# Performance work log

Measured on AMD Instinct MI355X. Metric: run time of the kernel, lower is better.

The kernel has to match this reference:

```python
import jax, jax.numpy as jnp
import numpy as np

WINSIZE = 11
SIGMA = 1.5
L_RANGE = 1.0

def _gaussian_window(winsize, channel, dtype=jnp.float32):
    x = jnp.arange(winsize, dtype=dtype)
    g = jnp.exp(-((x - winsize // 2) ** 2) / (2.0 * SIGMA ** 2))
    g = g / g.sum()
    w2d = jnp.outer(g, g)                      # [ws, ws]
    # depthwise kernel [channel, 1, ws, ws] (OIHW, feature_group_count=channel)
    return jnp.broadcast_to(w2d, (channel, 1, winsize, winsize))

def _dwconv(x, w, channel):
    pad = WINSIZE // 2
    return jax.lax.conv_general_dilated(
        x, w, window_strides=(1, 1), padding=[(pad, pad), (pad, pad)],
        dimension_numbers=('NCHW', 'OIHW', 'NCHW'),
        feature_group_count=channel)

def _ssim(X, Y):
    channel = X.shape[1]
    w = _gaussian_window(WINSIZE, channel, X.dtype)
    mu1 = _dwconv(X, w, channel)
    mu2 = _dwconv(Y, w, channel)
    mu1_sq = mu1 * mu1
    mu2_sq = mu2 * mu2
    mu1_mu2 = mu1 * mu2
    sigma1_sq = _dwconv(X * X, w, channel) - mu1_sq
    sigma2_sq = _dwconv(Y * Y, w, channel) - mu2_sq
    sigma12 = _dwconv(X * Y, w, channel) - mu1_mu2
    C1 = (0.01 * L_RANGE) ** 2
    C2 = (0.03 * L_RANGE) ** 2
    ssim_map = ((2.0 * mu1_mu2 + C1) * (2.0 * sigma12 + C2)) / \
               ((mu1_sq + mu2_sq + C1) * (sigma1_sq + sigma2_sq + C2))
    return jnp.mean(ssim_map)  # sizeavg=True

def setup_inputs() -> dict:
    key = jax.random.key(0)
    k1, k2 = jax.random.split(key)
    shape = (16, 3, 512, 512)
    X = jax.random.uniform(k1, shape, dtype=jnp.float32)
    Y = jax.random.uniform(k2, shape, dtype=jnp.float32)
    return {"X": X, "Y": Y}

def reference(X, Y):
    return 1.0 - _ssim(X, Y)
```

## Files before the change

### kernel.cpp

```cpp
#include <hip/hip_runtime.h>
#include <hip/hip_fp16.h>


#define ROWS 32
#define NI   (ROWS + 10)
#define NBLOCKS (48 * 16)
#define NPIXEL 12582912.0

__global__ __launch_bounds__(256) void ssim_pk_kernel(
    const float* __restrict__ X, const float* __restrict__ Y,
    float* __restrict__ partial)
{
    __shared__ __half2 sb[2][2][2][262];

    const int tid = threadIdx.x;
    const int bid = blockIdx.x;
    const int img = bid >> 4;
    const int r0  = (bid & 15) * ROWS;

    const float* __restrict__ Xi = X + (size_t)img * (512 * 512);
    const float* __restrict__ Yi = Y + (size_t)img * (512 * 512);

    float g[11];
    {
        float s = 0.f;
        #pragma unroll
        for (int i = 0; i < 11; ++i) {
            float d = (float)(i - 5);
            float e = expf(-d * d * (1.0f / 4.5f));
            g[i] = e; s += e;
        }
        float inv = 1.0f / s;
        #pragma unroll
        for (int i = 0; i < 11; ++i) g[i] *= inv;
    }
    __half2 w2[11];
    #pragma unroll
    for (int i = 0; i < 11; ++i) w2[i] = __float2half2_rn(g[i]);

    const __half2 hz = __float2half2_rn(0.f);

    if (tid < 2) {
        #pragma unroll
        for (int b = 0; b < 2; ++b)
            #pragma unroll
            for (int m = 0; m < 2; ++m) {
                sb[b][m][0][1 + tid]   = hz;
                sb[b][m][0][259 + tid] = hz;
                sb[b][m][1][tid]       = hz;
                sb[b][m][1][259 + tid] = hz;
            }
    }

    const int c2 = 2 * tid;

    {
        int gr = r0 - 5;
        float2 xv = {0.f, 0.f}, yv = {0.f, 0.f};
        float xn = 0.f, yn = 0.f;
        if ((unsigned)gr < 512u) {
            const float* xr = Xi + (size_t)gr * 512;
            const float* yr = Yi + (size_t)gr * 512;
            xv = *(const float2*)(xr + c2);
            yv = *(const float2*)(yr + c2);
            if (tid < 255) { xn = xr[c2 + 2]; yn = yr[c2 + 2]; }
        }
        sb[0][0][0][tid + 3] = __floats2half2_rn(xv.x, xv.y);
        sb[0][0][1][tid + 3] = __floats2half2_rn(xv.y, xn);
        sb[0][1][0][tid + 3] = __floats2half2_rn(yv.x, yv.y);
        sb[0][1][1][tid + 3] = __floats2half2_rn(yv.y, yn);
        if (tid == 0) {
            sb[0][0][1][2] = __floats2half2_rn(0.f, xv.x);
            sb[0][1][1][2] = __floats2half2_rn(0.f, yv.x);
        }
    }
    __syncthreads();

    __half2 ring[5][11];
    float acc = 0.f;
    const float C1 = 1e-4f, C2 = 9e-4f;

    #pragma unroll 1
    for (int jb = 0; jb < 44; jb += 11) {
        #pragma unroll
        for (int ph = 0; ph < 11; ++ph) {
            int j = jb + ph;
            if (j < NI) {
                const int cur = j & 1, nxt = cur ^ 1;
                const int jn = j + 1;

                float2 nxv = {0.f, 0.f}, nyv = {0.f, 0.f};
                float nxn = 0.f, nyn = 0.f;
                if (jn < NI) {
                    int gr = r0 - 5 + jn;
                    if ((unsigned)gr < 512u) {
                        const float* xr = Xi + (size_t)gr * 512;
                        const float* yr = Yi + (size_t)gr * 512;
                        nxv = *(const float2*)(xr + c2);
                        nyv = *(const float2*)(yr + c2);
                        if (tid < 255) { nxn = xr[c2 + 2]; nyn = yr[c2 + 2]; }
                    }
                }

                {
                    const __half2* ex = &sb[cur][0][0][tid];
                    const __half2* ox = &sb[cur][0][1][tid];
                    const __half2* ey = &sb[cur][1][0][tid];
                    const __half2* oy = &sb[cur][1][1][tid];
                    __half2 hx = hz, hy = hz, hxx = hz, hyy = hz, hxy = hz;
                    #pragma unroll
                    for (int k = 0; k < 11; ++k) {
                        __half2 xk = (k & 1) ? ex[(k + 1) >> 1] : ox[k >> 1];
                        __half2 yk = (k & 1) ? ey[(k + 1) >> 1] : oy[k >> 1];
                        __half2 wx = __hmul2(w2[k], xk);
                        __half2 wy = __hmul2(w2[k], yk);
                        hx  = __hadd2(hx, wx);
                        hy  = __hadd2(hy, wy);
                        hxx = __hfma2(wx, xk, hxx);
                        hyy = __hfma2(wy, yk, hyy);
                        hxy = __hfma2(wx, yk, hxy);
                    }
                    ring[0][ph] = hx;  ring[1][ph] = hy;
                    ring[2][ph] = hxx; ring[3][ph] = hyy; ring[4][ph] = hxy;
                }

                if (j >= 10) {
                    __half2 mu1 = hz, mu2 = hz, vxx = hz, vyy = hz, vxy = hz;
                    #pragma unroll
                    for (int k = 0; k < 11; ++k) {
                        const int s = (ph + 1 + k) % 11;
                        mu1 = __hfma2(w2[k], ring[0][s], mu1);
                        mu2 = __hfma2(w2[k], ring[1][s], mu2);
                        vxx = __hfma2(w2[k], ring[2][s], vxx);
                        vyy = __hfma2(w2[k], ring[3][s], vyy);
                        vxy = __hfma2(w2[k], ring[4][s], vxy);
                    }
                    float2 m1 = __half22float2(mu1);
                    float2 m2 = __half22float2(mu2);
                    float2 xx = __half22float2(vxx);
                    float2 yy = __half22float2(vyy);
                    float2 xy = __half22float2(vxy);
                    #pragma unroll
                    for (int h = 0; h < 2; ++h) {
                        float a1 = h ? m1.y : m1.x;
                        float a2 = h ? m2.y : m2.x;
                        float bx = h ? xx.y : xx.x;
                        float by = h ? yy.y : yy.x;
                        float bz = h ? xy.y : xy.x;
                        float m11 = a1 * a1, m22 = a2 * a2, m12 = a1 * a2;
                        float s1 = bx - m11, s2 = by - m22, s12 = bz - m12;
                        float num = (2.f * m12 + C1) * (2.f * s12 + C2);
                        float den = (m11 + m22 + C1) * (s1 + s2 + C2);
                        acc = fmaf(num, __builtin_amdgcn_rcpf(den), acc);
                    }
                }

                if (jn < NI) {
                    sb[nxt][0][0][tid + 3] = __floats2half2_rn(nxv.x, nxv.y);
                    sb[nxt][0][1][tid + 3] = __floats2half2_rn(nxv.y, nxn);
                    sb[nxt][1][0][tid + 3] = __floats2half2_rn(nyv.x, nyv.y);
                    sb[nxt][1][1][tid + 3] = __floats2half2_rn(nyv.y, nyn);
                    if (tid == 0) {
                        sb[nxt][0][1][2] = __floats2half2_rn(0.f, nxv.x);
                        sb[nxt][1][1][2] = __floats2half2_rn(0.f, nyv.x);
                    }
                }
                __syncthreads();
            }
        }
    }

    #pragma unroll
    for (int off = 32; off > 0; off >>= 1)
        acc += __shfl_down(acc, off, 64);

    __shared__ float wsum[4];
    const int lane = tid & 63, wid = tid >> 6;
    if (lane == 0) wsum[wid] = acc;
    __syncthreads();
    if (tid == 0)
        partial[bid] = wsum[0] + wsum[1] + wsum[2] + wsum[3];
}

__global__ __launch_bounds__(256) void ssim_reduce_kernel(
    const float* __restrict__ partial, float* __restrict__ out)
{
    const int tid = threadIdx.x;
    double s = 0.0;
    for (int i = tid; i < NBLOCKS; i += 256) s += (double)partial[i];
    __shared__ double sd[256];
    sd[tid] = s;
    __syncthreads();
    for (int off = 128; off > 0; off >>= 1) {
        if (tid < off) sd[tid] += sd[tid + off];
        __syncthreads();
    }
    if (tid == 0) out[0] = (float)(1.0 - sd[0] / NPIXEL);
}

extern "C" void kernel_launch(void* const* d_in, const int* in_sizes, int n_in,
                              void* d_out, int out_size, void* d_ws, size_t ws_size,
                              hipStream_t stream) {
    const float* X = (const float*)d_in[0];
    const float* Y = (const float*)d_in[1];
    float* partial = (float*)d_ws;
    float* out = (float*)d_out;

    ssim_pk_kernel<<<NBLOCKS, 256, 0, stream>>>(X, Y, partial);
    ssim_reduce_kernel<<<1, 256, 0, stream>>>(partial, out);
}
```

Baseline: 63.82 us.

## Split strips per wavefront with private LDS halos to drop block barriers

```diff
diff --git a/kernel.cpp b/kernel.cpp
--- a/kernel.cpp
+++ b/kernel.cpp
@@ -4,19 +4,34 @@
 
 #define ROWS 32
 #define NI   (ROWS + 10)
-#define NBLOCKS (48 * 16)
-#define NPIXEL 12582912.0
+#define NSTRIP 3072
+#define NBLK  (NSTRIP / 4)
+#define NPIX  12582912.0
 
-__global__ __launch_bounds__(256) void ssim_pk_kernel(
+static __device__ __forceinline__ unsigned fun16(unsigned hi, unsigned lo) {
+    return (unsigned)((((unsigned long long)hi << 32) | lo) >> 16);
+}
+static __device__ __forceinline__ unsigned h2u(__half2 v) {
+    unsigned u; __builtin_memcpy(&u, &v, 4); return u;
+}
+static __device__ __forceinline__ __half2 u2h(unsigned u) {
+    __half2 v; __builtin_memcpy(&v, &u, 4); return v;
+}
+
+__global__ __launch_bounds__(256, 3) void ssim_sweep_kernel(
     const float* __restrict__ X, const float* __restrict__ Y,
     float* __restrict__ partial)
 {
-    __shared__ __half2 sb[2][2][2][262];
+    __shared__ unsigned sbw[4][2][2][72];
 
-    const int tid = threadIdx.x;
-    const int bid = blockIdx.x;
-    const int img = bid >> 4;
-    const int r0  = (bid & 15) * ROWS;
+    const int tid  = threadIdx.x;
+    const int lane = tid & 63;
+    const int w    = tid >> 6;
+    const int sid  = blockIdx.x * 4 + w;
+    const int img  = sid >> 6;
+    const int rb   = (sid >> 2) & 15;
+    const int cs   = (sid & 3) << 7;
+    const int r0   = rb * ROWS;
 
     const float* __restrict__ Xi = X + (size_t)img * (512 * 512);
     const float* __restrict__ Yi = Y + (size_t)img * (512 * 512);
@@ -38,91 +53,79 @@
     #pragma unroll
     for (int i = 0; i < 11; ++i) w2[i] = __float2half2_rn(g[i]);
 
-    const __half2 hz = __float2half2_rn(0.f);
+    const int c2 = cs + 2 * lane;
 
-    if (tid < 2) {
-        #pragma unroll
-        for (int b = 0; b < 2; ++b)
-            #pragma unroll
-            for (int m = 0; m < 2; ++m) {
-                sb[b][m][0][1 + tid]   = hz;
-                sb[b][m][0][259 + tid] = hz;
-                sb[b][m][1][tid]       = hz;
-                sb[b][m][1][259 + tid] = hz;
-            }
-    }
+    int hq = -1, hm = 0;
+    if (lane >= 48 && lane < 54)      { hq = lane - 48; hm = 0; }
+    else if (lane >= 56 && lane < 62) { hq = lane - 56; hm = 1; }
+    const int  hwd = (hq < 0) ? 0 : (hq < 3 ? hq : 64 + hq);
+    const int  hc  = cs - 6 + 2 * hwd;
+    const bool hok = (hq >= 0) && ((unsigned)hc < 512u);
+    const float* hbase = hm ? Yi : Xi;
 
-    const int c2 = 2 * tid;
+    float2 nvx, nvy, nvh;
+    #define STAGE_LOAD(J)                                                    \
+        {                                                                    \
+            int gr = r0 - 5 + (J);                                           \
+            nvx = make_float2(0.f, 0.f); nvy = nvx; nvh = nvx;               \
+            if ((unsigned)gr < 512u) {                                       \
+                const float* xr = Xi + (size_t)gr * 512;                     \
+                const float* yr = Yi + (size_t)gr * 512;                     \
+                nvx = *(const float2*)(xr + c2);                             \
+                nvy = *(const float2*)(yr + c2);                             \
+                if (hok) nvh = *(const float2*)(hbase + (size_t)gr * 512 + hc); \
+            }                                                                \
+        }
+    #define STAGE_WRITE(BUF)                                                 \
+        {                                                                    \
+            sbw[w][0][BUF][3 + lane] = h2u(__floats2half2_rn(nvx.x, nvx.y)); \
+            sbw[w][1][BUF][3 + lane] = h2u(__floats2half2_rn(nvy.x, nvy.y)); \
+            if (hq >= 0) sbw[w][hm][BUF][hwd] = h2u(__floats2half2_rn(nvh.x, nvh.y)); \
+        }
 
-    {
-        int gr = r0 - 5;
-        float2 xv = {0.f, 0.f}, yv = {0.f, 0.f};
-        float xn = 0.f, yn = 0.f;
-        if ((unsigned)gr < 512u) {
-            const float* xr = Xi + (size_t)gr * 512;
-            const float* yr = Yi + (size_t)gr * 512;
-            xv = *(const float2*)(xr + c2);
-            yv = *(const float2*)(yr + c2);
-            if (tid < 255) { xn = xr[c2 + 2]; yn = yr[c2 + 2]; }
-        }
-        sb[0][0][0][tid + 3] = __floats2half2_rn(xv.x, xv.y);
-        sb[0][0][1][tid + 3] = __floats2half2_rn(xv.y, xn);
-        sb[0][1][0][tid + 3] = __floats2half2_rn(yv.x, yv.y);
-        sb[0][1][1][tid + 3] = __floats2half2_rn(yv.y, yn);
-        if (tid == 0) {
-            sb[0][0][1][2] = __floats2half2_rn(0.f, xv.x);
-            sb[0][1][1][2] = __floats2half2_rn(0.f, yv.x);
-        }
-    }
-    __syncthreads();
+    STAGE_LOAD(0);
+    STAGE_WRITE(0);
+    asm volatile("s_waitcnt lgkmcnt(0)" ::: "memory");
 
     __half2 ring[5][11];
     float acc = 0.f;
     const float C1 = 1e-4f, C2 = 9e-4f;
+    const __half2 hz = __float2half2_rn(0.f);
 
     #pragma unroll 1
     for (int jb = 0; jb < 44; jb += 11) {
         #pragma unroll
         for (int ph = 0; ph < 11; ++ph) {
-            int j = jb + ph;
+            const int j = jb + ph;
             if (j < NI) {
                 const int cur = j & 1, nxt = cur ^ 1;
-                const int jn = j + 1;
 
-                float2 nxv = {0.f, 0.f}, nyv = {0.f, 0.f};
-                float nxn = 0.f, nyn = 0.f;
-                if (jn < NI) {
-                    int gr = r0 - 5 + jn;
-                    if ((unsigned)gr < 512u) {
-                        const float* xr = Xi + (size_t)gr * 512;
-                        const float* yr = Yi + (size_t)gr * 512;
-                        nxv = *(const float2*)(xr + c2);
-                        nyv = *(const float2*)(yr + c2);
-                        if (tid < 255) { nxn = xr[c2 + 2]; nyn = yr[c2 + 2]; }
-                    }
+                if (j + 1 < NI) STAGE_LOAD(j + 1);
+
+                unsigned Dx[7], Dy[7];
+                #pragma unroll
+                for (int k2 = 0; k2 < 7; ++k2) Dx[k2] = sbw[w][0][cur][lane + k2];
+                #pragma unroll
+                for (int k2 = 0; k2 < 7; ++k2) Dy[k2] = sbw[w][1][cur][lane + k2];
+
+                __half2 hx = hz, hy = hz, hxx = hz, hyy = hz, hxy = hz;
+                #pragma unroll
+                for (int k = 0; k < 11; ++k) {
+                    unsigned ux, uy;
+                    if (k & 1) { ux = Dx[(k + 1) >> 1];            uy = Dy[(k + 1) >> 1]; }
+                    else       { ux = fun16(Dx[(k >> 1) + 1], Dx[k >> 1]);
+                                 uy = fun16(Dy[(k >> 1) + 1], Dy[k >> 1]); }
+                    __half2 xk = u2h(ux), yk = u2h(uy);
+                    __half2 wx = __hmul2(w2[k], xk);
+                    __half2 wy = __hmul2(w2[k], yk);
+                    hx  = __hadd2(hx, wx);
+                    hy  = __hadd2(hy, wy);
+                    hxx = __hfma2(wx, xk, hxx);
+                    hyy = __hfma2(wy, yk, hyy);
+                    hxy = __hfma2(wx, yk, hxy);
                 }
-
-                {
-                    const __half2* ex = &sb[cur][0][0][tid];
-                    const __half2* ox = &sb[cur][0][1][tid];
-                    const __half2* ey = &sb[cur][1][0][tid];
-                    const __half2* oy = &sb[cur][1][1][tid];
-                    __half2 hx = hz, hy = hz, hxx = hz, hyy = hz, hxy = hz;
-                    #pragma unroll
-                    for (int k = 0; k < 11; ++k) {
-                        __half2 xk = (k & 1) ? ex[(k + 1) >> 1] : ox[k >> 1];
-                        __half2 yk = (k & 1) ? ey[(k + 1) >> 1] : oy[k >> 1];
-                        __half2 wx = __hmul2(w2[k], xk);
-                        __half2 wy = __hmul2(w2[k], yk);
-                        hx  = __hadd2(hx, wx);
-                        hy  = __hadd2(hy, wy);
-                        hxx = __hfma2(wx, xk, hxx);
-                        hyy = __hfma2(wy, yk, hyy);
-                        hxy = __hfma2(wx, yk, hxy);
-                    }
-                    ring[0][ph] = hx;  ring[1][ph] = hy;
-                    ring[2][ph] = hxx; ring[3][ph] = hyy; ring[4][ph] = hxy;
-                }
+                ring[0][ph] = hx;  ring[1][ph] = hy;
+                ring[2][ph] = hxx; ring[3][ph] = hyy; ring[4][ph] = hxy;
 
                 if (j >= 10) {
                     __half2 mu1 = hz, mu2 = hz, vxx = hz, vyy = hz, vxy = hz;
@@ -155,17 +158,8 @@
                     }
                 }
 
-                if (jn < NI) {
-                    sb[nxt][0][0][tid + 3] = __floats2half2_rn(nxv.x, nxv.y);
-                    sb[nxt][0][1][tid + 3] = __floats2half2_rn(nxv.y, nxn);
-                    sb[nxt][1][0][tid + 3] = __floats2half2_rn(nyv.x, nyv.y);
-                    sb[nxt][1][1][tid + 3] = __floats2half2_rn(nyv.y, nyn);
-                    if (tid == 0) {
-                        sb[nxt][0][1][2] = __floats2half2_rn(0.f, nxv.x);
-                        sb[nxt][1][1][2] = __floats2half2_rn(0.f, nyv.x);
-                    }
-                }
-                __syncthreads();
+                if (j + 1 < NI) STAGE_WRITE(nxt);
+                asm volatile("s_waitcnt lgkmcnt(0)" ::: "memory");
             }
         }
     }
@@ -173,13 +167,7 @@
     #pragma unroll
     for (int off = 32; off > 0; off >>= 1)
         acc += __shfl_down(acc, off, 64);
-
-    __shared__ float wsum[4];
-    const int lane = tid & 63, wid = tid >> 6;
-    if (lane == 0) wsum[wid] = acc;
-    __syncthreads();
-    if (tid == 0)
-        partial[bid] = wsum[0] + wsum[1] + wsum[2] + wsum[3];
+    if (lane == 0) partial[sid] = acc;
 }
 
 __global__ __launch_bounds__(256) void ssim_reduce_kernel(
@@ -187,7 +175,7 @@
 {
     const int tid = threadIdx.x;
     double s = 0.0;
-    for (int i = tid; i < NBLOCKS; i += 256) s += (double)partial[i];
+    for (int i = tid; i < NSTRIP; i += 256) s += (double)partial[i];
     __shared__ double sd[256];
     sd[tid] = s;
     __syncthreads();
@@ -195,7 +183,7 @@
         if (tid < off) sd[tid] += sd[tid + off];
         __syncthreads();
     }
-    if (tid == 0) out[0] = (float)(1.0 - sd[0] / NPIXEL);
+    if (tid == 0) out[0] = (float)(1.0 - sd[0] / NPIX);
 }
 
 extern "C" void kernel_launch(void* const* d_in, const int* in_sizes, int n_in,
@@ -206,6 +194,6 @@
     float* partial = (float*)d_ws;
     float* out = (float*)d_out;
 
-    ssim_pk_kernel<<<NBLOCKS, 256, 0, stream>>>(X, Y, partial);
+    ssim_sweep_kernel<<<NBLK, 256, 0, stream>>>(X, Y, partial);
     ssim_reduce_kernel<<<1, 256, 0, stream>>>(partial, out);
 }
```

New measurement: 61.19 us. 4.1% less time.
